# Kernel tuning notes

Hardware: AMD Instinct MI355X
Metric: run time of the kernel (lower is better)

The kernel has to match this reference:

```python
import jax, jax.numpy as jnp
import numpy as np

N = 100000   # nodes
E = 1600000  # edges (avg degree 16)
D = 128      # input feature dim
H = 128      # Config.hidden_dim
G = 64       # graphs in batch
OUT = 2      # output classes


def setup_inputs() -> dict:
    key = jax.random.key(0)
    ks = jax.random.split(key, 12)
    s = 0.05
    return {
        "x": jax.random.normal(ks[0], (N, D), dtype=jnp.float32),
        "edge_index": jax.random.randint(ks[1], (2, E), 0, N),
        "batch": jnp.sort(jax.random.randint(ks[2], (N,), 0, G)),
        "W1": jax.random.normal(ks[3], (H, D), dtype=jnp.float32) * s,
        "b1": jnp.zeros((H,), jnp.float32),
        "W2": jax.random.normal(ks[4], (H, H), dtype=jnp.float32) * s,
        "b2": jnp.zeros((H,), jnp.float32),
        "Wf1": jax.random.normal(ks[5], (H, H), dtype=jnp.float32) * s,
        "bf1": jnp.zeros((H,), jnp.float32),
        "Wf2": jax.random.normal(ks[6], (OUT, H), dtype=jnp.float32) * s,
        "bf2": jnp.zeros((OUT,), jnp.float32),
    }


def _gnn_layer(x, src, dst, W, b):
    # message(x_j) = Linear(x[src]); linear commutes with gather, so transform
    # node features once (N rows) instead of per-edge (E rows): same math.
    xw = x @ W.T + b                                   # [N, H]
    msg = xw[src]                                      # [E, H] gather
    summed = jax.ops.segment_sum(msg, dst, num_segments=N)            # [N, H]
    cnt = jax.ops.segment_sum(jnp.ones((src.shape[0],), x.dtype), dst,
                              num_segments=N)                          # [N]
    return summed / jnp.maximum(cnt, 1.0)[:, None]     # scatter-mean (0 for deg-0)


def reference(x, edge_index, batch, W1, b1, W2, b2, Wf1, bf1, Wf2, bf2):
    src, dst = edge_index[0], edge_index[1]
    h = jax.nn.relu(_gnn_layer(x, src, dst, W1, b1))
    h = jax.nn.relu(_gnn_layer(h, src, dst, W2, b2))
    g = jax.ops.segment_max(h, batch, num_segments=G)  # global_max_pool [G, H]
    z = jax.nn.relu(g @ Wf1.T + bf1)                   # fc (dropout = identity, eval)
    z = z @ Wf2.T + bf2                                # [G, OUT]
    return jax.nn.log_softmax(z, axis=1)
```

## Files before the change

kernel.cpp:

```cpp
#include <hip/hip_runtime.h>
#include <hip/hip_fp16.h>
#include <math.h>


#define SPLIT 64
#define BUCKET_SHIFT 8
#define BUCKET_SIZE 256
#define MAXBUCK 512
#define BIN_CHUNK 4096
#define CAP 4608
#define LSTR 136

typedef _Float16 half8 __attribute__((ext_vector_type(8)));
typedef _Float16 half4v __attribute__((ext_vector_type(4)));
typedef _Float16 half2v __attribute__((ext_vector_type(2)));
typedef float floatx4 __attribute__((ext_vector_type(4)));
typedef float floatx2 __attribute__((ext_vector_type(2)));

#define RFL(v) __builtin_amdgcn_readfirstlane(v)

__global__ void k_init(int* __restrict__ bcur, int* __restrict__ gstart,
                       int* __restrict__ gend,
                       const float* __restrict__ W1, const float* __restrict__ W2,
                       _Float16* __restrict__ w1h, _Float16* __restrict__ w2h,
                       int G, int nbuck) {
    int i = blockIdx.x * blockDim.x + threadIdx.x;
    if (i < nbuck) bcur[i] = i * CAP;
    if (i < G) { gstart[i] = 0; gend[i] = 0; }
    w1h[i] = (_Float16)W1[i];
    w2h[i] = (_Float16)W2[i];
}

__global__ __launch_bounds__(256) void k_bin(
        const int* __restrict__ src, const int* __restrict__ dst,
        int* __restrict__ bcur, int* __restrict__ staging,
        const int* __restrict__ batch, int* __restrict__ gstart,
        int* __restrict__ gend, int E, int N, int nbuck) {
    __shared__ int lh[MAXBUCK];
    __shared__ int lbase[MAXBUCK];
    __shared__ int lc[MAXBUCK];
    int t = threadIdx.x;
    for (int i = t; i < nbuck; i += 256) { lh[i] = 0; lc[i] = 0; }

    int n = blockIdx.x * 256 + t;
    if (n < N) {
        int b = batch[n];
        if (n == 0 || batch[n - 1] != b) gstart[b] = n;
        if (n == N - 1 || batch[n + 1] != b) gend[b] = n + 1;
    }
    __syncthreads();

    int base = blockIdx.x * BIN_CHUNK;
    if (base + BIN_CHUNK <= E) {
        int ds[16], ss[16];
        const int4* dv = (const int4*)(dst + base);
        const int4* sv = (const int4*)(src + base);
        #pragma unroll
        for (int j = 0; j < 4; ++j) {
            int4 d = dv[j * 256 + t];
            int4 s = sv[j * 256 + t];
            ds[j * 4 + 0] = d.x; ds[j * 4 + 1] = d.y;
            ds[j * 4 + 2] = d.z; ds[j * 4 + 3] = d.w;
            ss[j * 4 + 0] = s.x; ss[j * 4 + 1] = s.y;
            ss[j * 4 + 2] = s.z; ss[j * 4 + 3] = s.w;
        }
        #pragma unroll
        for (int q = 0; q < 16; ++q)
            atomicAdd(&lh[ds[q] >> BUCKET_SHIFT], 1);
        __syncthreads();
        for (int i = t; i < nbuck; i += 256)
            if (lh[i]) lbase[i] = atomicAdd(&bcur[i], lh[i]);
        __syncthreads();
        #pragma unroll
        for (int q = 0; q < 16; ++q) {
            int d = ds[q];
            int b = d >> BUCKET_SHIFT;
            int pos = lbase[b] + atomicAdd(&lc[b], 1);
            if (pos < (b + 1) * CAP)
                staging[pos] = ss[q] | ((d & (BUCKET_SIZE - 1)) << 24);
        }
    } else {
        for (int e = base + t; e < E; e += 256)
            atomicAdd(&lh[dst[e] >> BUCKET_SHIFT], 1);
        __syncthreads();
        for (int i = t; i < nbuck; i += 256)
            if (lh[i]) lbase[i] = atomicAdd(&bcur[i], lh[i]);
        __syncthreads();
        for (int e = base + t; e < E; e += 256) {
            int d = dst[e];
            int b = d >> BUCKET_SHIFT;
            int pos = lbase[b] + atomicAdd(&lc[b], 1);
            if (pos < (b + 1) * CAP)
                staging[pos] = src[e] | ((d & (BUCKET_SIZE - 1)) << 24);
        }
    }
}

__global__ __launch_bounds__(BUCKET_SIZE) void k_bcsr(
        const int* __restrict__ staging, const int* __restrict__ bcur,
        int* __restrict__ esrc, int* __restrict__ rowstart,
        int* __restrict__ deg, int N) {
    __shared__ int sw[CAP];
    __shared__ int lh[BUCKET_SIZE];
    __shared__ int lcur[BUCKET_SIZE];
    __shared__ int wsum[4];
    int b = blockIdx.x;
    int s = b * CAP;
    int e = min(bcur[b], s + CAP);
    int len = e - s;
    int t = threadIdx.x;
    lh[t] = 0;
    __syncthreads();
    for (int i = t; i < len; i += BUCKET_SIZE) {
        int p = staging[s + i];
        sw[i] = p;
        atomicAdd(&lh[((unsigned)p) >> 24], 1);
    }
    __syncthreads();
    int v = lh[t];
    int lane = t & 63;
    int wv = t >> 6;
    int inc = v;
    #pragma unroll
    for (int off = 1; off < 64; off <<= 1) {
        int x = __shfl_up(inc, off, 64);
        if (lane >= off) inc += x;
    }
    if (lane == 63) wsum[wv] = inc;
    __syncthreads();
    int woff = 0;
    #pragma unroll
    for (int k = 0; k < 3; ++k)
        if (k < wv) woff += wsum[k];
    int excl = woff + inc - v;
    int node = b * BUCKET_SIZE + t;
    if (node < N) { rowstart[node] = s + excl; deg[node] = v; }
    lcur[t] = excl;
    __syncthreads();
    for (int i = t; i < len; i += BUCKET_SIZE) {
        int p = sw[i];
        int local = ((unsigned)p) >> 24;
        int pos = atomicAdd(&lcur[local], 1);
        esrc[s + pos] = p & 0xFFFFFF;
    }
}

template <typename T>
__global__ __launch_bounds__(512) void k_gemm(const T* __restrict__ in,
                                              const _Float16* __restrict__ Wh,
                                              const float* __restrict__ bias,
                                              unsigned char* __restrict__ out8,
                                              int N) {
    __shared__ _Float16 sX[128 * LSTR];
    __shared__ _Float16 sW[128 * LSTR];
    int t = threadIdx.x;

    #pragma unroll
    for (int it = 0; it < 8; ++it) {
        int lin = it * 512 + t;
        int r = lin >> 5;
        int c = (lin & 31) * 4;
        *(half4v*)&sW[r * LSTR + c] = *(const half4v*)(Wh + r * 128 + c);
    }

    int w = t >> 6;
    int lane = t & 63;
    int quad = lane >> 4;
    int lrow = lane & 15;

    #pragma unroll
    for (int tile = 0; tile < 2; ++tile) {
        int n0 = blockIdx.x * 256 + tile * 128;
        __syncthreads();
        #pragma unroll
        for (int it = 0; it < 8; ++it) {
            int lin = it * 512 + t;
            int r = lin >> 5;
            int c = (lin & 31) * 4;
            half4v xh;
            int n = n0 + r;
            if (n < N) {
                if constexpr (sizeof(T) == 4) {
                    float4 xv = *(const float4*)((const float*)in + (size_t)n * 128 + c);
                    xh = half4v{ (_Float16)xv.x, (_Float16)xv.y, (_Float16)xv.z, (_Float16)xv.w };
                } else {
                    xh = *(const half4v*)((const _Float16*)in + (size_t)n * 128 + c);
                }
            } else {
                xh = half4v{ 0, 0, 0, 0 };
            }
            *(half4v*)&sX[r * LSTR + c] = xh;
        }
        __syncthreads();

        floatx4 acc[8];
        #pragma unroll
        for (int i = 0; i < 8; ++i) acc[i] = {0.f, 0.f, 0.f, 0.f};

        int arow = (w * 16 + lrow) * LSTR + quad * 8;
        #pragma unroll
        for (int k0 = 0; k0 < 128; k0 += 32) {
            half8 a = *(const half8*)&sX[arow + k0];
            #pragma unroll
            for (int ht = 0; ht < 8; ++ht) {
                half8 bfr = *(const half8*)&sW[(ht * 16 + lrow) * LSTR + quad * 8 + k0];
                acc[ht] = __builtin_amdgcn_mfma_f32_16x16x32_f16(a, bfr, acc[ht], 0, 0, 0);
            }
        }

        #pragma unroll
        for (int ht = 0; ht < 8; ++ht) {
            int h = ht * 16 + lrow;
            float bv = bias[h];
            #pragma unroll
            for (int r = 0; r < 4; ++r) {
                int node = n0 + w * 16 + quad * 4 + r;
                if (node < N) {
                    float v = acc[ht][r] + bv;
                    int pk = __builtin_amdgcn_cvt_pk_fp8_f32(v, v, 0, false);
                    out8[(size_t)node * 128 + h] = (unsigned char)(pk & 0xFF);
                }
            }
        }
    }
}

__global__ __launch_bounds__(256) void k_agg(const unsigned char* __restrict__ in8,
                                             const int* __restrict__ esrc,
                                             const int* __restrict__ rowstart,
                                             const int* __restrict__ deg,
                                             _Float16* __restrict__ outh, int N) {
    int lane = threadIdx.x & 63;
    int node = blockIdx.x * 4 + (threadIdx.x >> 6);
    if (node >= N) return;
    int start = RFL(rowstart[node]);
    int d     = RFL(deg[node]);
    const unsigned short* in16 = (const unsigned short*)in8;

    floatx2 a0 = {0.f, 0.f}, a1 = {0.f, 0.f}, a2 = {0.f, 0.f}, a3 = {0.f, 0.f};

    int i = 0;
    for (; i + 8 <= d; i += 8) {
        int x0 = RFL(esrc[start + i + 0]);
        int x1 = RFL(esrc[start + i + 1]);
        int x2 = RFL(esrc[start + i + 2]);
        int x3 = RFL(esrc[start + i + 3]);
        int x4 = RFL(esrc[start + i + 4]);
        int x5 = RFL(esrc[start + i + 5]);
        int x6 = RFL(esrc[start + i + 6]);
        int x7 = RFL(esrc[start + i + 7]);
        unsigned u0 = in16[((size_t)x0 << 6) + lane];
        unsigned u1 = in16[((size_t)x1 << 6) + lane];
        unsigned u2 = in16[((size_t)x2 << 6) + lane];
        unsigned u3 = in16[((size_t)x3 << 6) + lane];
        unsigned u4 = in16[((size_t)x4 << 6) + lane];
        unsigned u5 = in16[((size_t)x5 << 6) + lane];
        unsigned u6 = in16[((size_t)x6 << 6) + lane];
        unsigned u7 = in16[((size_t)x7 << 6) + lane];
        floatx2 f0 = __builtin_amdgcn_cvt_pk_f32_fp8(u0, false);
        floatx2 f1 = __builtin_amdgcn_cvt_pk_f32_fp8(u1, false);
        floatx2 f2 = __builtin_amdgcn_cvt_pk_f32_fp8(u2, false);
        floatx2 f3 = __builtin_amdgcn_cvt_pk_f32_fp8(u3, false);
        floatx2 f4 = __builtin_amdgcn_cvt_pk_f32_fp8(u4, false);
        floatx2 f5 = __builtin_amdgcn_cvt_pk_f32_fp8(u5, false);
        floatx2 f6 = __builtin_amdgcn_cvt_pk_f32_fp8(u6, false);
        floatx2 f7 = __builtin_amdgcn_cvt_pk_f32_fp8(u7, false);
        a0.x += f0.x; a0.y += f0.y;  a1.x += f1.x; a1.y += f1.y;
        a2.x += f2.x; a2.y += f2.y;  a3.x += f3.x; a3.y += f3.y;
        a0.x += f4.x; a0.y += f4.y;  a1.x += f5.x; a1.y += f5.y;
        a2.x += f6.x; a2.y += f6.y;  a3.x += f7.x; a3.y += f7.y;
    }
    for (; i + 4 <= d; i += 4) {
        int x0 = RFL(esrc[start + i + 0]);
        int x1 = RFL(esrc[start + i + 1]);
        int x2 = RFL(esrc[start + i + 2]);
        int x3 = RFL(esrc[start + i + 3]);
        unsigned u0 = in16[((size_t)x0 << 6) + lane];
        unsigned u1 = in16[((size_t)x1 << 6) + lane];
        unsigned u2 = in16[((size_t)x2 << 6) + lane];
        unsigned u3 = in16[((size_t)x3 << 6) + lane];
        floatx2 f0 = __builtin_amdgcn_cvt_pk_f32_fp8(u0, false);
        floatx2 f1 = __builtin_amdgcn_cvt_pk_f32_fp8(u1, false);
        floatx2 f2 = __builtin_amdgcn_cvt_pk_f32_fp8(u2, false);
        floatx2 f3 = __builtin_amdgcn_cvt_pk_f32_fp8(u3, false);
        a0.x += f0.x; a0.y += f0.y;  a1.x += f1.x; a1.y += f1.y;
        a2.x += f2.x; a2.y += f2.y;  a3.x += f3.x; a3.y += f3.y;
    }
    for (; i < d; ++i) {
        int x0 = RFL(esrc[start + i]);
        unsigned u0 = in16[((size_t)x0 << 6) + lane];
        floatx2 f0 = __builtin_amdgcn_cvt_pk_f32_fp8(u0, false);
        a0.x += f0.x; a0.y += f0.y;
    }

    float sx = (a0.x + a1.x) + (a2.x + a3.x);
    float sy = (a0.y + a1.y) + (a2.y + a3.y);
    float dm = fmaxf((float)d, 1.0f);
    half2v r = { (_Float16)fmaxf(sx / dm, 0.f),
                 (_Float16)fmaxf(sy / dm, 0.f) };
    *(half2v*)(outh + (size_t)node * 128 + lane * 2) = r;
}

__global__ void k_pool1(const _Float16* __restrict__ h, const int* __restrict__ gstart,
                        const int* __restrict__ gend, float* __restrict__ pm, int G) {
    int g = blockIdx.x / SPLIT;
    int c = blockIdx.x % SPLIT;
    int t = threadIdx.x;
    int s = gstart[g], e = gend[g];
    int len = e - s;
    int chunk = (len + SPLIT - 1) / SPLIT;
    int lo = s + c * chunk;
    int hi = min(lo + chunk, e);
    float m = -INFINITY;
    int n = lo;
    for (; n + 8 <= hi; n += 8) {
        float v0 = (float)h[(size_t)(n + 0) * 128 + t];
        float v1 = (float)h[(size_t)(n + 1) * 128 + t];
        float v2 = (float)h[(size_t)(n + 2) * 128 + t];
        float v3 = (float)h[(size_t)(n + 3) * 128 + t];
        float v4 = (float)h[(size_t)(n + 4) * 128 + t];
        float v5 = (float)h[(size_t)(n + 5) * 128 + t];
        float v6 = (float)h[(size_t)(n + 6) * 128 + t];
        float v7 = (float)h[(size_t)(n + 7) * 128 + t];
        float m0 = fmaxf(fmaxf(v0, v1), fmaxf(v2, v3));
        float m1 = fmaxf(fmaxf(v4, v5), fmaxf(v6, v7));
        m = fmaxf(m, fmaxf(m0, m1));
    }
    for (; n < hi; ++n)
        m = fmaxf(m, (float)h[(size_t)n * 128 + t]);
    pm[((size_t)g * SPLIT + c) * 128 + t] = m;
}

__global__ void k_fc(const float* __restrict__ pm,
                     const float* __restrict__ Wf1, const float* __restrict__ bf1,
                     const float* __restrict__ Wf2, const float* __restrict__ bf2,
                     float* __restrict__ out) {
    __shared__ float sg[128];
    __shared__ float sz[128];
    __shared__ float so[2];
    int g = blockIdx.x;
    int t = threadIdx.x;
    float m = -INFINITY;
    #pragma unroll 8
    for (int c = 0; c < SPLIT; ++c)
        m = fmaxf(m, pm[((size_t)g * SPLIT + c) * 128 + t]);
    sg[t] = m;
    __syncthreads();
    float z = bf1[t];
    #pragma unroll 4
    for (int d = 0; d < 128; ++d)
        z += sg[d] * Wf1[t * 128 + d];
    sz[t] = fmaxf(z, 0.f);
    __syncthreads();
    if (t < 2) {
        float o = bf2[t];
        for (int d = 0; d < 128; ++d)
            o += sz[d] * Wf2[t * 128 + d];
        so[t] = o;
    }
    __syncthreads();
    if (t == 0) {
        float a = so[0], b = so[1];
        float mx = fmaxf(a, b);
        float ls = mx + logf(expf(a - mx) + expf(b - mx));
        out[g * 2 + 0] = a - ls;
        out[g * 2 + 1] = b - ls;
    }
}

extern "C" void kernel_launch(void* const* d_in, const int* in_sizes, int n_in,
                              void* d_out, int out_size, void* d_ws, size_t ws_size,
                              hipStream_t stream) {
    const float* x   = (const float*)d_in[0];
    const int*   ei  = (const int*)d_in[1];
    const int* batch = (const int*)d_in[2];
    const float* W1  = (const float*)d_in[3];
    const float* b1  = (const float*)d_in[4];
    const float* W2  = (const float*)d_in[5];
    const float* b2  = (const float*)d_in[6];
    const float* Wf1 = (const float*)d_in[7];
    const float* bf1 = (const float*)d_in[8];
    const float* Wf2 = (const float*)d_in[9];
    const float* bf2 = (const float*)d_in[10];

    int N = in_sizes[2];
    int E = in_sizes[1] / 2;
    int G = out_size / 2;
    const int* src = ei;
    const int* dst = ei + E;
    int nbuck = (N + BUCKET_SIZE - 1) / BUCKET_SIZE;

    char* p = (char*)d_ws;
    auto alloc = [&](size_t bytes) -> char* {
        char* r = p;
        p += (bytes + 255) & ~(size_t)255;
        return r;
    };
    unsigned char* A = (unsigned char*)alloc((size_t)N * 128);
    _Float16* B    = (_Float16*)alloc((size_t)N * 128 * 2);
    int* deg       = (int*)alloc((size_t)N * 4);
    int* rowstart  = (int*)alloc((size_t)N * 4);
    int* esrc      = (int*)alloc((size_t)nbuck * CAP * 4);
    int* staging   = (int*)alloc((size_t)nbuck * CAP * 4);
    int* bcur      = (int*)alloc((MAXBUCK + 2) * 4);
    int* gstart    = (int*)alloc((size_t)G * 4);
    int* gend      = (int*)alloc((size_t)G * 4);
    float* pm      = (float*)alloc((size_t)G * SPLIT * 128 * 4);
    _Float16* w1h  = (_Float16*)alloc((size_t)128 * 128 * 2);
    _Float16* w2h  = (_Float16*)alloc((size_t)128 * 128 * 2);

    int nchunk = (E + BIN_CHUNK - 1) / BIN_CHUNK;

    k_init<<<64, 256, 0, stream>>>(bcur, gstart, gend, W1, W2, w1h, w2h, G, nbuck);
    k_bin<<<nchunk, 256, 0, stream>>>(src, dst, bcur, staging, batch,
                                      gstart, gend, E, N, nbuck);
    k_bcsr<<<nbuck, BUCKET_SIZE, 0, stream>>>(staging, bcur, esrc, rowstart, deg, N);

    k_gemm<float><<<(N + 255) / 256, 512, 0, stream>>>(x, w1h, b1, A, N);
    k_agg<<<(N + 3) / 4, 256, 0, stream>>>(A, esrc, rowstart, deg, B, N);
    k_gemm<_Float16><<<(N + 255) / 256, 512, 0, stream>>>(B, w2h, b2, A, N);
    k_agg<<<(N + 3) / 4, 256, 0, stream>>>(A, esrc, rowstart, deg, B, N);
    k_pool1<<<G * SPLIT, 128, 0, stream>>>(B, gstart, gend, pm, G);
    k_fc<<<G, 128, 0, stream>>>(pm, Wf1, bf1, Wf2, bf2, (float*)d_out);
}
```

Measured before the change: 291.0 us.

## Fuse first aggregation with second layer GEMM into one kernel

Adds a kernel that gathers and scatter-means neighbour features for 128 nodes into shared memory, applies ReLU, then runs the MFMA tile for the second linear layer. This removes the fp16 intermediate B write and read between the first aggregation and the second GEMM, and one kernel launch. The GEMM also drops the shared-memory weight staging and reads weights straight from global memory/cache, uses 128-node blocks, and sets an occupancy hint. Risks: each wave serially handles 16 nodes, so there is less latency hiding than with one node per wave, and the weight loads go through global memory.

Result: slower. 347.9 us (+19.6%).

```diff
diff --git a/kernel.cpp b/kernel.cpp
--- a/kernel.cpp
+++ b/kernel.cpp
@@ -145,84 +145,160 @@
     }
 }
 
-template <typename T>
-__global__ __launch_bounds__(512) void k_gemm(const T* __restrict__ in,
-                                              const _Float16* __restrict__ Wh,
-                                              const float* __restrict__ bias,
-                                              unsigned char* __restrict__ out8,
-                                              int N) {
+__device__ __forceinline__ void mfma_tile(const _Float16* sX,
+                                          const _Float16* __restrict__ Wh,
+                                          const float* __restrict__ bias,
+                                          unsigned char* __restrict__ out8,
+                                          int n0, int N, int t) {
+    int w = t >> 6;
+    int lane = t & 63;
+    int quad = lane >> 4;
+    int lrow = lane & 15;
+
+    floatx4 acc[8];
+    #pragma unroll
+    for (int i = 0; i < 8; ++i) acc[i] = {0.f, 0.f, 0.f, 0.f};
+
+    int arow = (w * 16 + lrow) * LSTR + quad * 8;
+    #pragma unroll
+    for (int k0 = 0; k0 < 128; k0 += 32) {
+        half8 a = *(const half8*)&sX[arow + k0];
+        #pragma unroll
+        for (int ht = 0; ht < 8; ++ht) {
+            half8 b = *(const half8*)(Wh + (ht * 16 + lrow) * 128 + quad * 8 + k0);
+            acc[ht] = __builtin_amdgcn_mfma_f32_16x16x32_f16(a, b, acc[ht], 0, 0, 0);
+        }
+    }
+
+    #pragma unroll
+    for (int ht = 0; ht < 8; ++ht) {
+        int h = ht * 16 + lrow;
+        float bv = bias[h];
+        #pragma unroll
+        for (int r = 0; r < 4; ++r) {
+            int node = n0 + w * 16 + quad * 4 + r;
+            if (node < N) {
+                float v = acc[ht][r] + bv;
+                int pk = __builtin_amdgcn_cvt_pk_fp8_f32(v, v, 0, false);
+                out8[(size_t)node * 128 + h] = (unsigned char)(pk & 0xFF);
+            }
+        }
+    }
+}
+
+__global__ __launch_bounds__(512, 6) void k_gemm(const float* __restrict__ in,
+                                                 const _Float16* __restrict__ Wh,
+                                                 const float* __restrict__ bias,
+                                                 unsigned char* __restrict__ out8,
+                                                 int N) {
     __shared__ _Float16 sX[128 * LSTR];
-    __shared__ _Float16 sW[128 * LSTR];
     int t = threadIdx.x;
+    int n0 = blockIdx.x * 128;
 
     #pragma unroll
     for (int it = 0; it < 8; ++it) {
         int lin = it * 512 + t;
         int r = lin >> 5;
         int c = (lin & 31) * 4;
-        *(half4v*)&sW[r * LSTR + c] = *(const half4v*)(Wh + r * 128 + c);
-    }
-
+        half4v xh = {0, 0, 0, 0};
+        int n = n0 + r;
+        if (n < N) {
+            float4 xv = *(const float4*)(in + (size_t)n * 128 + c);
+            xh = half4v{ (_Float16)xv.x, (_Float16)xv.y, (_Float16)xv.z, (_Float16)xv.w };
+        }
+        *(half4v*)&sX[r * LSTR + c] = xh;
+    }
+    __syncthreads();
+    mfma_tile(sX, Wh, bias, out8, n0, N, t);
+}
+
+__global__ __launch_bounds__(512, 6) void k_ag(const unsigned char* __restrict__ in8,
+                                               const int* __restrict__ esrc,
+                                               const int* __restrict__ rowstart,
+                                               const int* __restrict__ deg,
+                                               const _Float16* __restrict__ Wh,
+                                               const float* __restrict__ bias,
+                                               unsigned char* __restrict__ out8,
+                                               int N) {
+    __shared__ _Float16 sX[128 * LSTR];
+    int t = threadIdx.x;
     int w = t >> 6;
     int lane = t & 63;
-    int quad = lane >> 4;
-    int lrow = lane & 15;
-
-    #pragma unroll
-    for (int tile = 0; tile < 2; ++tile) {
-        int n0 = blockIdx.x * 256 + tile * 128;
-        __syncthreads();
-        #pragma unroll
-        for (int it = 0; it < 8; ++it) {
-            int lin = it * 512 + t;
-            int r = lin >> 5;
-            int c = (lin & 31) * 4;
-            half4v xh;
-            int n = n0 + r;
-            if (n < N) {
-                if constexpr (sizeof(T) == 4) {
-                    float4 xv = *(const float4*)((const float*)in + (size_t)n * 128 + c);
-                    xh = half4v{ (_Float16)xv.x, (_Float16)xv.y, (_Float16)xv.z, (_Float16)xv.w };
-                } else {
-                    xh = *(const half4v*)((const _Float16*)in + (size_t)n * 128 + c);
-                }
-            } else {
-                xh = half4v{ 0, 0, 0, 0 };
+    int n0 = blockIdx.x * 128;
+    const unsigned short* in16 = (const unsigned short*)in8;
+
+    for (int k = 0; k < 16; ++k) {
+        int node = n0 + w * 16 + k;
+        float sx = 0.f, sy = 0.f;
+        int dd = 0;
+        if (node < N) {
+            int start = RFL(rowstart[node]);
+            int d     = RFL(deg[node]);
+            dd = d;
+            floatx2 a0 = {0.f, 0.f}, a1 = {0.f, 0.f}, a2 = {0.f, 0.f}, a3 = {0.f, 0.f};
+            int i = 0;
+            for (; i + 8 <= d; i += 8) {
+                int x0 = RFL(esrc[start + i + 0]);
+                int x1 = RFL(esrc[start + i + 1]);
+                int x2 = RFL(esrc[start + i + 2]);
+                int x3 = RFL(esrc[start + i + 3]);
+                int x4 = RFL(esrc[start + i + 4]);
+                int x5 = RFL(esrc[start + i + 5]);
+                int x6 = RFL(esrc[start + i + 6]);
+                int x7 = RFL(esrc[start + i + 7]);
+                unsigned u0 = in16[((size_t)x0 << 6) + lane];
+                unsigned u1 = in16[((size_t)x1 << 6) + lane];
+                unsigned u2 = in16[((size_t)x2 << 6) + lane];
+                unsigned u3 = in16[((size_t)x3 << 6) + lane];
+                unsigned u4 = in16[((size_t)x4 << 6) + lane];
+                unsigned u5 = in16[((size_t)x5 << 6) + lane];
+                unsigned u6 = in16[((size_t)x6 << 6) + lane];
+                unsigned u7 = in16[((size_t)x7 << 6) + lane];
+                floatx2 f0 = __builtin_amdgcn_cvt_pk_f32_fp8(u0, false);
+                floatx2 f1 = __builtin_amdgcn_cvt_pk_f32_fp8(u1, false);
+                floatx2 f2 = __builtin_amdgcn_cvt_pk_f32_fp8(u2, false);
+                floatx2 f3 = __builtin_amdgcn_cvt_pk_f32_fp8(u3, false);
+                floatx2 f4 = __builtin_amdgcn_cvt_pk_f32_fp8(u4, false);
+                floatx2 f5 = __builtin_amdgcn_cvt_pk_f32_fp8(u5, false);
+                floatx2 f6 = __builtin_amdgcn_cvt_pk_f32_fp8(u6, false);
+                floatx2 f7 = __builtin_amdgcn_cvt_pk_f32_fp8(u7, false);
+                a0.x += f0.x; a0.y += f0.y;  a1.x += f1.x; a1.y += f1.y;
+                a2.x += f2.x; a2.y += f2.y;  a3.x += f3.x; a3.y += f3.y;
+                a0.x += f4.x; a0.y += f4.y;  a1.x += f5.x; a1.y += f5.y;
+                a2.x += f6.x; a2.y += f6.y;  a3.x += f7.x; a3.y += f7.y;
             }
-            *(half4v*)&sX[r * LSTR + c] = xh;
-        }
-        __syncthreads();
-
-        floatx4 acc[8];
-        #pragma unroll
-        for (int i = 0; i < 8; ++i) acc[i] = {0.f, 0.f, 0.f, 0.f};
-
-        int arow = (w * 16 + lrow) * LSTR + quad * 8;
-        #pragma unroll
-        for (int k0 = 0; k0 < 128; k0 += 32) {
-            half8 a = *(const half8*)&sX[arow + k0];
-            #pragma unroll
-            for (int ht = 0; ht < 8; ++ht) {
-                half8 bfr = *(const half8*)&sW[(ht * 16 + lrow) * LSTR + quad * 8 + k0];
-                acc[ht] = __builtin_amdgcn_mfma_f32_16x16x32_f16(a, bfr, acc[ht], 0, 0, 0);
+            for (; i + 4 <= d; i += 4) {
+                int x0 = RFL(esrc[start + i + 0]);
+                int x1 = RFL(esrc[start + i + 1]);
+                int x2 = RFL(esrc[start + i + 2]);
+                int x3 = RFL(esrc[start + i + 3]);
+                unsigned u0 = in16[((size_t)x0 << 6) + lane];
+                unsigned u1 = in16[((size_t)x1 << 6) + lane];
+                unsigned u2 = in16[((size_t)x2 << 6) + lane];
+                unsigned u3 = in16[((size_t)x3 << 6) + lane];
+                floatx2 f0 = __builtin_amdgcn_cvt_pk_f32_fp8(u0, false);
+                floatx2 f1 = __builtin_amdgcn_cvt_pk_f32_fp8(u1, false);
+                floatx2 f2 = __builtin_amdgcn_cvt_pk_f32_fp8(u2, false);
+                floatx2 f3 = __builtin_amdgcn_cvt_pk_f32_fp8(u3, false);
+                a0.x += f0.x; a0.y += f0.y;  a1.x += f1.x; a1.y += f1.y;
+                a2.x += f2.x; a2.y += f2.y;  a3.x += f3.x; a3.y += f3.y;
             }
-        }
-
-        #pragma unroll
-        for (int ht = 0; ht < 8; ++ht) {
-            int h = ht * 16 + lrow;
-            float bv = bias[h];
-            #pragma unroll
-            for (int r = 0; r < 4; ++r) {
-                int node = n0 + w * 16 + quad * 4 + r;
-                if (node < N) {
-                    float v = acc[ht][r] + bv;
-                    int pk = __builtin_amdgcn_cvt_pk_fp8_f32(v, v, 0, false);
-                    out8[(size_t)node * 128 + h] = (unsigned char)(pk & 0xFF);
-                }
+            for (; i < d; ++i) {
+                int x0 = RFL(esrc[start + i]);
+                unsigned u0 = in16[((size_t)x0 << 6) + lane];
+                floatx2 f0 = __builtin_amdgcn_cvt_pk_f32_fp8(u0, false);
+                a0.x += f0.x; a0.y += f0.y;
             }
-        }
-    }
+            sx = (a0.x + a1.x) + (a2.x + a3.x);
+            sy = (a0.y + a1.y) + (a2.y + a3.y);
+        }
+        float dm = fmaxf((float)dd, 1.0f);
+        half2v hv = { (_Float16)fmaxf(sx / dm, 0.f),
+                      (_Float16)fmaxf(sy / dm, 0.f) };
+        *(half2v*)&sX[(w * 16 + k) * LSTR + lane * 2] = hv;
+    }
+    __syncthreads();
+    mfma_tile(sX, Wh, bias, out8, n0, N, t);
 }
 
 __global__ __launch_bounds__(256) void k_agg(const unsigned char* __restrict__ in8,
@@ -396,7 +472,8 @@
         p += (bytes + 255) & ~(size_t)255;
         return r;
     };
-    unsigned char* A = (unsigned char*)alloc((size_t)N * 128);
+    unsigned char* A  = (unsigned char*)alloc((size_t)N * 128);
+    unsigned char* A2 = (unsigned char*)alloc((size_t)N * 128);
     _Float16* B    = (_Float16*)alloc((size_t)N * 128 * 2);
     int* deg       = (int*)alloc((size_t)N * 4);
     int* rowstart  = (int*)alloc((size_t)N * 4);
@@ -416,10 +493,9 @@
                                       gstart, gend, E, N, nbuck);
     k_bcsr<<<nbuck, BUCKET_SIZE, 0, stream>>>(staging, bcur, esrc, rowstart, deg, N);
 
-    k_gemm<float><<<(N + 255) / 256, 512, 0, stream>>>(x, w1h, b1, A, N);
-    k_agg<<<(N + 3) / 4, 256, 0, stream>>>(A, esrc, rowstart, deg, B, N);
-    k_gemm<_Float16><<<(N + 255) / 256, 512, 0, stream>>>(B, w2h, b2, A, N);
-    k_agg<<<(N + 3) / 4, 256, 0, stream>>>(A, esrc, rowstart, deg, B, N);
+    k_gemm<<<(N + 127) / 128, 512, 0, stream>>>(x, w1h, b1, A, N);
+    k_ag<<<(N + 127) / 128, 512, 0, stream>>>(A, esrc, rowstart, deg, w2h, b2, A2, N);
+    k_agg<<<(N + 3) / 4, 256, 0, stream>>>(A2, esrc, rowstart, deg, B, N);
     k_pool1<<<G * SPLIT, 128, 0, stream>>>(B, gstart, gend, pm, G);
     k_fc<<<G, 128, 0, stream>>>(pm, Wf1, bf1, Wf2, bf2, (float*)d_out);
 }
```

## Fuse GEMM, aggregation, pooling and FC stages into one cooperative persistent kernel

Applied to the files above, without the earlier changes.

Replaces the six separate launches (two GEMMs, two aggregations, pooling, FC) with a single cooperative kernel that loops over tiles and nodes in grid-stride fashion and separates stages with grid.sync. The GEMM no longer stages W in shared memory; it reads B fragments straight from global/L2, which halves LDS use so more blocks fit per CU. A second fp8 buffer avoids reusing A between layers. This removes launch gaps and tail effects, but adds grid-wide barriers and caps residency, which may reduce latency hiding for the gather-bound aggregation.

After: 695.7 us. +139.1%, slower.

```diff
diff --git a/kernel.cpp b/kernel.cpp
--- a/kernel.cpp
+++ b/kernel.cpp
@@ -1,4 +1,5 @@
 #include <hip/hip_runtime.h>
+#include <hip/hip_cooperative_groups.h>
 #include <hip/hip_fp16.h>
 #include <math.h>
 
@@ -18,6 +19,8 @@
 typedef float floatx2 __attribute__((ext_vector_type(2)));
 
 #define RFL(v) __builtin_amdgcn_readfirstlane(v)
+
+namespace cg = cooperative_groups;
 
 __global__ void k_init(int* __restrict__ bcur, int* __restrict__ gstart,
                        int* __restrict__ gend,
@@ -145,100 +148,78 @@
     }
 }
 
+
 template <typename T>
-__global__ __launch_bounds__(512) void k_gemm(const T* __restrict__ in,
-                                              const _Float16* __restrict__ Wh,
-                                              const float* __restrict__ bias,
-                                              unsigned char* __restrict__ out8,
-                                              int N) {
-    __shared__ _Float16 sX[128 * LSTR];
-    __shared__ _Float16 sW[128 * LSTR];
-    int t = threadIdx.x;
-
+__device__ __forceinline__ void gemm_tile(const T* __restrict__ in,
+                                          const _Float16* __restrict__ Wh,
+                                          const float* __restrict__ bias,
+                                          unsigned char* __restrict__ out8,
+                                          int n0, int N, int t, _Float16* sX) {
     #pragma unroll
     for (int it = 0; it < 8; ++it) {
         int lin = it * 512 + t;
         int r = lin >> 5;
         int c = (lin & 31) * 4;
-        *(half4v*)&sW[r * LSTR + c] = *(const half4v*)(Wh + r * 128 + c);
-    }
+        half4v xh = {0, 0, 0, 0};
+        int n = n0 + r;
+        if (n < N) {
+            if constexpr (sizeof(T) == 4) {
+                float4 xv = *(const float4*)((const float*)in + (size_t)n * 128 + c);
+                xh = half4v{ (_Float16)xv.x, (_Float16)xv.y, (_Float16)xv.z, (_Float16)xv.w };
+            } else {
+                xh = *(const half4v*)((const _Float16*)in + (size_t)n * 128 + c);
+            }
+        }
+        *(half4v*)&sX[r * LSTR + c] = xh;
+    }
+    __syncthreads();
 
     int w = t >> 6;
     int lane = t & 63;
     int quad = lane >> 4;
     int lrow = lane & 15;
 
-    #pragma unroll
-    for (int tile = 0; tile < 2; ++tile) {
-        int n0 = blockIdx.x * 256 + tile * 128;
-        __syncthreads();
-        #pragma unroll
-        for (int it = 0; it < 8; ++it) {
-            int lin = it * 512 + t;
-            int r = lin >> 5;
-            int c = (lin & 31) * 4;
-            half4v xh;
-            int n = n0 + r;
-            if (n < N) {
-                if constexpr (sizeof(T) == 4) {
-                    float4 xv = *(const float4*)((const float*)in + (size_t)n * 128 + c);
-                    xh = half4v{ (_Float16)xv.x, (_Float16)xv.y, (_Float16)xv.z, (_Float16)xv.w };
-                } else {
-                    xh = *(const half4v*)((const _Float16*)in + (size_t)n * 128 + c);
-                }
-            } else {
-                xh = half4v{ 0, 0, 0, 0 };
-            }
-            *(half4v*)&sX[r * LSTR + c] = xh;
-        }
-        __syncthreads();
-
-        floatx4 acc[8];
-        #pragma unroll
-        for (int i = 0; i < 8; ++i) acc[i] = {0.f, 0.f, 0.f, 0.f};
-
-        int arow = (w * 16 + lrow) * LSTR + quad * 8;
-        #pragma unroll
-        for (int k0 = 0; k0 < 128; k0 += 32) {
-            half8 a = *(const half8*)&sX[arow + k0];
-            #pragma unroll
-            for (int ht = 0; ht < 8; ++ht) {
-                half8 bfr = *(const half8*)&sW[(ht * 16 + lrow) * LSTR + quad * 8 + k0];
-                acc[ht] = __builtin_amdgcn_mfma_f32_16x16x32_f16(a, bfr, acc[ht], 0, 0, 0);
-            }
-        }
-
+    floatx4 acc[8];
+    #pragma unroll
+    for (int i = 0; i < 8; ++i) acc[i] = {0.f, 0.f, 0.f, 0.f};
+
+    int arow = (w * 16 + lrow) * LSTR + quad * 8;
+    #pragma unroll
+    for (int k0 = 0; k0 < 128; k0 += 32) {
+        half8 a = *(const half8*)&sX[arow + k0];
         #pragma unroll
         for (int ht = 0; ht < 8; ++ht) {
-            int h = ht * 16 + lrow;
-            float bv = bias[h];
-            #pragma unroll
-            for (int r = 0; r < 4; ++r) {
-                int node = n0 + w * 16 + quad * 4 + r;
-                if (node < N) {
-                    float v = acc[ht][r] + bv;
-                    int pk = __builtin_amdgcn_cvt_pk_fp8_f32(v, v, 0, false);
-                    out8[(size_t)node * 128 + h] = (unsigned char)(pk & 0xFF);
-                }
+            half8 b = *(const half8*)(Wh + (ht * 16 + lrow) * 128 + quad * 8 + k0);
+            acc[ht] = __builtin_amdgcn_mfma_f32_16x16x32_f16(a, b, acc[ht], 0, 0, 0);
+        }
+    }
+
+    #pragma unroll
+    for (int ht = 0; ht < 8; ++ht) {
+        int h = ht * 16 + lrow;
+        float bv = bias[h];
+        #pragma unroll
+        for (int r = 0; r < 4; ++r) {
+            int node = n0 + w * 16 + quad * 4 + r;
+            if (node < N) {
+                float v = acc[ht][r] + bv;
+                int pk = __builtin_amdgcn_cvt_pk_fp8_f32(v, v, 0, false);
+                out8[(size_t)node * 128 + h] = (unsigned char)(pk & 0xFF);
             }
         }
     }
-}
-
-__global__ __launch_bounds__(256) void k_agg(const unsigned char* __restrict__ in8,
-                                             const int* __restrict__ esrc,
-                                             const int* __restrict__ rowstart,
-                                             const int* __restrict__ deg,
-                                             _Float16* __restrict__ outh, int N) {
-    int lane = threadIdx.x & 63;
-    int node = blockIdx.x * 4 + (threadIdx.x >> 6);
-    if (node >= N) return;
+    __syncthreads();
+}
+
+__device__ __forceinline__ void agg_one(const unsigned short* __restrict__ in16,
+                                        const int* __restrict__ esrc,
+                                        const int* __restrict__ rowstart,
+                                        const int* __restrict__ deg,
+                                        int lane, int node,
+                                        _Float16* __restrict__ outh) {
     int start = RFL(rowstart[node]);
     int d     = RFL(deg[node]);
-    const unsigned short* in16 = (const unsigned short*)in8;
-
     floatx2 a0 = {0.f, 0.f}, a1 = {0.f, 0.f}, a2 = {0.f, 0.f}, a3 = {0.f, 0.f};
-
     int i = 0;
     for (; i + 8 <= d; i += 8) {
         int x0 = RFL(esrc[start + i + 0]);
@@ -292,7 +273,6 @@
         floatx2 f0 = __builtin_amdgcn_cvt_pk_f32_fp8(u0, false);
         a0.x += f0.x; a0.y += f0.y;
     }
-
     float sx = (a0.x + a1.x) + (a2.x + a3.x);
     float sy = (a0.y + a1.y) + (a2.y + a3.y);
     float dm = fmaxf((float)d, 1.0f);
@@ -301,70 +281,117 @@
     *(half2v*)(outh + (size_t)node * 128 + lane * 2) = r;
 }
 
-__global__ void k_pool1(const _Float16* __restrict__ h, const int* __restrict__ gstart,
-                        const int* __restrict__ gend, float* __restrict__ pm, int G) {
-    int g = blockIdx.x / SPLIT;
-    int c = blockIdx.x % SPLIT;
+__global__ __launch_bounds__(512, 6) void k_net(
+        const float* __restrict__ x,
+        const _Float16* __restrict__ w1h, const float* __restrict__ b1,
+        const _Float16* __restrict__ w2h, const float* __restrict__ b2,
+        const float* __restrict__ Wf1, const float* __restrict__ bf1,
+        const float* __restrict__ Wf2, const float* __restrict__ bf2,
+        const int* __restrict__ esrc, const int* __restrict__ rowstart,
+        const int* __restrict__ deg, const int* __restrict__ gstart,
+        const int* __restrict__ gend,
+        unsigned char* __restrict__ A, unsigned char* __restrict__ A2,
+        _Float16* __restrict__ B, float* __restrict__ pm,
+        float* __restrict__ out, int N, int G) {
+    cg::grid_group grid = cg::this_grid();
+    __shared__ _Float16 sX[128 * LSTR];
     int t = threadIdx.x;
-    int s = gstart[g], e = gend[g];
-    int len = e - s;
-    int chunk = (len + SPLIT - 1) / SPLIT;
-    int lo = s + c * chunk;
-    int hi = min(lo + chunk, e);
-    float m = -INFINITY;
-    int n = lo;
-    for (; n + 8 <= hi; n += 8) {
-        float v0 = (float)h[(size_t)(n + 0) * 128 + t];
-        float v1 = (float)h[(size_t)(n + 1) * 128 + t];
-        float v2 = (float)h[(size_t)(n + 2) * 128 + t];
-        float v3 = (float)h[(size_t)(n + 3) * 128 + t];
-        float v4 = (float)h[(size_t)(n + 4) * 128 + t];
-        float v5 = (float)h[(size_t)(n + 5) * 128 + t];
-        float v6 = (float)h[(size_t)(n + 6) * 128 + t];
-        float v7 = (float)h[(size_t)(n + 7) * 128 + t];
-        float m0 = fmaxf(fmaxf(v0, v1), fmaxf(v2, v3));
-        float m1 = fmaxf(fmaxf(v4, v5), fmaxf(v6, v7));
-        m = fmaxf(m, fmaxf(m0, m1));
-    }
-    for (; n < hi; ++n)
-        m = fmaxf(m, (float)h[(size_t)n * 128 + t]);
-    pm[((size_t)g * SPLIT + c) * 128 + t] = m;
-}
-
-__global__ void k_fc(const float* __restrict__ pm,
-                     const float* __restrict__ Wf1, const float* __restrict__ bf1,
-                     const float* __restrict__ Wf2, const float* __restrict__ bf2,
-                     float* __restrict__ out) {
-    __shared__ float sg[128];
-    __shared__ float sz[128];
-    __shared__ float so[2];
-    int g = blockIdx.x;
-    int t = threadIdx.x;
-    float m = -INFINITY;
-    #pragma unroll 8
-    for (int c = 0; c < SPLIT; ++c)
-        m = fmaxf(m, pm[((size_t)g * SPLIT + c) * 128 + t]);
-    sg[t] = m;
-    __syncthreads();
-    float z = bf1[t];
-    #pragma unroll 4
-    for (int d = 0; d < 128; ++d)
-        z += sg[d] * Wf1[t * 128 + d];
-    sz[t] = fmaxf(z, 0.f);
-    __syncthreads();
-    if (t < 2) {
-        float o = bf2[t];
-        for (int d = 0; d < 128; ++d)
-            o += sz[d] * Wf2[t * 128 + d];
-        so[t] = o;
-    }
-    __syncthreads();
-    if (t == 0) {
-        float a = so[0], b = so[1];
-        float mx = fmaxf(a, b);
-        float ls = mx + logf(expf(a - mx) + expf(b - mx));
-        out[g * 2 + 0] = a - ls;
-        out[g * 2 + 1] = b - ls;
+    int nb = gridDim.x;
+    int ntile = (N + 127) >> 7;
+    int lane = t & 63;
+    int gw = ((blockIdx.x << 9) + t) >> 6;
+    int nw = (nb << 9) >> 6;
+
+    for (int tile = blockIdx.x; tile < ntile; tile += nb)
+        gemm_tile<float>(x, w1h, b1, A, tile << 7, N, t, sX);
+    grid.sync();
+
+    {
+        const unsigned short* in16 = (const unsigned short*)A;
+        for (int node = gw; node < N; node += nw)
+            agg_one(in16, esrc, rowstart, deg, lane, node, B);
+    }
+    grid.sync();
+
+    for (int tile = blockIdx.x; tile < ntile; tile += nb)
+        gemm_tile<_Float16>(B, w2h, b2, A2, tile << 7, N, t, sX);
+    grid.sync();
+
+    {
+        const unsigned short* in16 = (const unsigned short*)A2;
+        for (int node = gw; node < N; node += nw)
+            agg_one(in16, esrc, rowstart, deg, lane, node, B);
+    }
+    grid.sync();
+
+    {
+        int q = t >> 7;
+        int tt = t & 127;
+        for (int task = (blockIdx.x << 2) + q; task < G * SPLIT; task += nb << 2) {
+            int g = task >> 6;
+            int c = task & (SPLIT - 1);
+            int s = gstart[g], e = gend[g];
+            int len = e - s;
+            int chunk = (len + SPLIT - 1) / SPLIT;
+            int lo = s + c * chunk;
+            int hi = min(lo + chunk, e);
+            float m = -INFINITY;
+            int n = lo;
+            for (; n + 8 <= hi; n += 8) {
+                float v0 = (float)B[(size_t)(n + 0) * 128 + tt];
+                float v1 = (float)B[(size_t)(n + 1) * 128 + tt];
+                float v2 = (float)B[(size_t)(n + 2) * 128 + tt];
+                float v3 = (float)B[(size_t)(n + 3) * 128 + tt];
+                float v4 = (float)B[(size_t)(n + 4) * 128 + tt];
+                float v5 = (float)B[(size_t)(n + 5) * 128 + tt];
+                float v6 = (float)B[(size_t)(n + 6) * 128 + tt];
+                float v7 = (float)B[(size_t)(n + 7) * 128 + tt];
+                float m0 = fmaxf(fmaxf(v0, v1), fmaxf(v2, v3));
+                float m1 = fmaxf(fmaxf(v4, v5), fmaxf(v6, v7));
+                m = fmaxf(m, fmaxf(m0, m1));
+            }
+            for (; n < hi; ++n)
+                m = fmaxf(m, (float)B[(size_t)n * 128 + tt]);
+            pm[((size_t)g * SPLIT + c) * 128 + tt] = m;
+        }
+    }
+    grid.sync();
+
+    if (blockIdx.x < G) {
+        float* sg = (float*)sX;
+        float* sz = sg + 128;
+        float* so = sz + 128;
+        int g = blockIdx.x;
+        if (t < 128) {
+            float m = -INFINITY;
+            #pragma unroll 8
+            for (int c = 0; c < SPLIT; ++c)
+                m = fmaxf(m, pm[((size_t)g * SPLIT + c) * 128 + t]);
+            sg[t] = m;
+        }
+        __syncthreads();
+        if (t < 128) {
+            float z = bf1[t];
+            #pragma unroll 4
+            for (int d2 = 0; d2 < 128; ++d2)
+                z += sg[d2] * Wf1[t * 128 + d2];
+            sz[t] = fmaxf(z, 0.f);
+        }
+        __syncthreads();
+        if (t < 2) {
+            float o = bf2[t];
+            for (int d2 = 0; d2 < 128; ++d2)
+                o += sz[d2] * Wf2[t * 128 + d2];
+            so[t] = o;
+        }
+        __syncthreads();
+        if (t == 0) {
+            float a = so[0], b = so[1];
+            float mx = fmaxf(a, b);
+            float ls = mx + logf(expf(a - mx) + expf(b - mx));
+            out[g * 2 + 0] = a - ls;
+            out[g * 2 + 1] = b - ls;
+        }
     }
 }
 
@@ -396,7 +423,8 @@
         p += (bytes + 255) & ~(size_t)255;
         return r;
     };
-    unsigned char* A = (unsigned char*)alloc((size_t)N * 128);
+    unsigned char* A  = (unsigned char*)alloc((size_t)N * 128);
+    unsigned char* A2 = (unsigned char*)alloc((size_t)N * 128);
     _Float16* B    = (_Float16*)alloc((size_t)N * 128 * 2);
     int* deg       = (int*)alloc((size_t)N * 4);
     int* rowstart  = (int*)alloc((size_t)N * 4);
@@ -408,6 +436,7 @@
     float* pm      = (float*)alloc((size_t)G * SPLIT * 128 * 4);
     _Float16* w1h  = (_Float16*)alloc((size_t)128 * 128 * 2);
     _Float16* w2h  = (_Float16*)alloc((size_t)128 * 128 * 2);
+    float* outp    = (float*)d_out;
 
     int nchunk = (E + BIN_CHUNK - 1) / BIN_CHUNK;
 
@@ -416,10 +445,21 @@
                                       gstart, gend, E, N, nbuck);
     k_bcsr<<<nbuck, BUCKET_SIZE, 0, stream>>>(staging, bcur, esrc, rowstart, deg, N);
 
-    k_gemm<float><<<(N + 255) / 256, 512, 0, stream>>>(x, w1h, b1, A, N);
-    k_agg<<<(N + 3) / 4, 256, 0, stream>>>(A, esrc, rowstart, deg, B, N);
-    k_gemm<_Float16><<<(N + 255) / 256, 512, 0, stream>>>(B, w2h, b2, A, N);
-    k_agg<<<(N + 3) / 4, 256, 0, stream>>>(A, esrc, rowstart, deg, B, N);
-    k_pool1<<<G * SPLIT, 128, 0, stream>>>(B, gstart, gend, pm, G);
-    k_fc<<<G, 128, 0, stream>>>(pm, Wf1, bf1, Wf2, bf2, (float*)d_out);
-}
+    static int coopBlocks = 0;
+    if (coopBlocks == 0) {
+        int bpc = 0;
+        hipOccupancyMaxActiveBlocksPerMultiprocessor(&bpc, k_net, 512, 0);
+        if (bpc < 1) bpc = 1;
+        coopBlocks = bpc * 256;
+        if (coopBlocks > 1024) coopBlocks = 1024;
+    }
+    void* args[] = {
+        (void*)&x, (void*)&w1h, (void*)&b1, (void*)&w2h, (void*)&b2,
+        (void*)&Wf1, (void*)&bf1, (void*)&Wf2, (void*)&bf2,
+        (void*)&esrc, (void*)&rowstart, (void*)&deg, (void*)&gstart, (void*)&gend,
+        (void*)&A, (void*)&A2, (void*)&B, (void*)&pm, (void*)&outp,
+        (void*)&N, (void*)&G
+    };
+    hipLaunchCooperativeKernel((void*)k_net, dim3(coopBlocks), dim3(512),
+                               args, 0, stream);
+}
```

## Fuse first-layer GEMM into edge binning kernel as extra blocks

Applied to the files above, without the earlier changes.

Merges the edge binning kernel and the first-layer node GEMM into one launch, where the first blocks bin edges and the remaining blocks run the x@W1 transform. The two independent jobs can then overlap on the GPU and one kernel launch is removed. The binning part moves to 512-thread blocks with 8 edges per thread. The GEMM now uses one 128-row tile per block and reads W fragments straight from global/L2 instead of staging them in LDS. A separate output buffer A2 is added for the second layer.

Result: slower. 319.6 us (+9.8%).

```diff
diff --git a/kernel.cpp b/kernel.cpp
--- a/kernel.cpp
+++ b/kernel.cpp
@@ -31,67 +31,130 @@
     w2h[i] = (_Float16)W2[i];
 }
 
-__global__ __launch_bounds__(256) void k_bin(
+__global__ __launch_bounds__(512) void k_binG(
         const int* __restrict__ src, const int* __restrict__ dst,
         int* __restrict__ bcur, int* __restrict__ staging,
         const int* __restrict__ batch, int* __restrict__ gstart,
-        int* __restrict__ gend, int E, int N, int nbuck) {
-    __shared__ int lh[MAXBUCK];
-    __shared__ int lbase[MAXBUCK];
-    __shared__ int lc[MAXBUCK];
+        int* __restrict__ gend,
+        const float* __restrict__ x, const _Float16* __restrict__ w1h,
+        const float* __restrict__ b1, unsigned char* __restrict__ A,
+        int E, int N, int nbuck, int nchunk) {
+    __shared__ char smem_raw[128 * LSTR * 2];
     int t = threadIdx.x;
-    for (int i = t; i < nbuck; i += 256) { lh[i] = 0; lc[i] = 0; }
-
-    int n = blockIdx.x * 256 + t;
-    if (n < N) {
-        int b = batch[n];
-        if (n == 0 || batch[n - 1] != b) gstart[b] = n;
-        if (n == N - 1 || batch[n + 1] != b) gend[b] = n + 1;
-    }
-    __syncthreads();
-
-    int base = blockIdx.x * BIN_CHUNK;
-    if (base + BIN_CHUNK <= E) {
-        int ds[16], ss[16];
-        const int4* dv = (const int4*)(dst + base);
-        const int4* sv = (const int4*)(src + base);
-        #pragma unroll
-        for (int j = 0; j < 4; ++j) {
-            int4 d = dv[j * 256 + t];
-            int4 s = sv[j * 256 + t];
-            ds[j * 4 + 0] = d.x; ds[j * 4 + 1] = d.y;
-            ds[j * 4 + 2] = d.z; ds[j * 4 + 3] = d.w;
-            ss[j * 4 + 0] = s.x; ss[j * 4 + 1] = s.y;
-            ss[j * 4 + 2] = s.z; ss[j * 4 + 3] = s.w;
-        }
-        #pragma unroll
-        for (int q = 0; q < 16; ++q)
-            atomicAdd(&lh[ds[q] >> BUCKET_SHIFT], 1);
+
+    if (blockIdx.x < nchunk) {
+        int* lh    = (int*)smem_raw;
+        int* lbase = lh + MAXBUCK;
+        int* lc    = lbase + MAXBUCK;
+        if (t < MAXBUCK) { lh[t] = 0; lc[t] = 0; }
+
+        if (t < 256) {
+            int n = blockIdx.x * 256 + t;
+            if (n < N) {
+                int b = batch[n];
+                if (n == 0 || batch[n - 1] != b) gstart[b] = n;
+                if (n == N - 1 || batch[n + 1] != b) gend[b] = n + 1;
+            }
+        }
         __syncthreads();
-        for (int i = t; i < nbuck; i += 256)
-            if (lh[i]) lbase[i] = atomicAdd(&bcur[i], lh[i]);
+
+        int base = blockIdx.x * BIN_CHUNK;
+        if (base + BIN_CHUNK <= E) {
+            int ds[8], ss[8];
+            const int4* dv = (const int4*)(dst + base);
+            const int4* sv = (const int4*)(src + base);
+            #pragma unroll
+            for (int j = 0; j < 2; ++j) {
+                int4 d = dv[j * 512 + t];
+                int4 s = sv[j * 512 + t];
+                ds[j * 4 + 0] = d.x; ds[j * 4 + 1] = d.y;
+                ds[j * 4 + 2] = d.z; ds[j * 4 + 3] = d.w;
+                ss[j * 4 + 0] = s.x; ss[j * 4 + 1] = s.y;
+                ss[j * 4 + 2] = s.z; ss[j * 4 + 3] = s.w;
+            }
+            #pragma unroll
+            for (int q = 0; q < 8; ++q)
+                atomicAdd(&lh[ds[q] >> BUCKET_SHIFT], 1);
+            __syncthreads();
+            for (int i = t; i < nbuck; i += 512)
+                if (lh[i]) lbase[i] = atomicAdd(&bcur[i], lh[i]);
+            __syncthreads();
+            #pragma unroll
+            for (int q = 0; q < 8; ++q) {
+                int d = ds[q];
+                int b = d >> BUCKET_SHIFT;
+                int pos = lbase[b] + atomicAdd(&lc[b], 1);
+                if (pos < (b + 1) * CAP)
+                    staging[pos] = ss[q] | ((d & (BUCKET_SIZE - 1)) << 24);
+            }
+        } else {
+            for (int e = base + t; e < E; e += 512)
+                atomicAdd(&lh[dst[e] >> BUCKET_SHIFT], 1);
+            __syncthreads();
+            for (int i = t; i < nbuck; i += 512)
+                if (lh[i]) lbase[i] = atomicAdd(&bcur[i], lh[i]);
+            __syncthreads();
+            for (int e = base + t; e < E; e += 512) {
+                int d = dst[e];
+                int b = d >> BUCKET_SHIFT;
+                int pos = lbase[b] + atomicAdd(&lc[b], 1);
+                if (pos < (b + 1) * CAP)
+                    staging[pos] = src[e] | ((d & (BUCKET_SIZE - 1)) << 24);
+            }
+        }
+    } else {
+        _Float16* sX = (_Float16*)smem_raw;
+        int n0 = (blockIdx.x - nchunk) * 128;
+
+        #pragma unroll
+        for (int it = 0; it < 8; ++it) {
+            int lin = it * 512 + t;
+            int r = lin >> 5;
+            int c = (lin & 31) * 4;
+            half4v xh = {0, 0, 0, 0};
+            int n = n0 + r;
+            if (n < N) {
+                float4 xv = *(const float4*)(x + (size_t)n * 128 + c);
+                xh = half4v{ (_Float16)xv.x, (_Float16)xv.y,
+                             (_Float16)xv.z, (_Float16)xv.w };
+            }
+            *(half4v*)&sX[r * LSTR + c] = xh;
+        }
         __syncthreads();
-        #pragma unroll
-        for (int q = 0; q < 16; ++q) {
-            int d = ds[q];
-            int b = d >> BUCKET_SHIFT;
-            int pos = lbase[b] + atomicAdd(&lc[b], 1);
-            if (pos < (b + 1) * CAP)
-                staging[pos] = ss[q] | ((d & (BUCKET_SIZE - 1)) << 24);
-        }
-    } else {
-        for (int e = base + t; e < E; e += 256)
-            atomicAdd(&lh[dst[e] >> BUCKET_SHIFT], 1);
-        __syncthreads();
-        for (int i = t; i < nbuck; i += 256)
-            if (lh[i]) lbase[i] = atomicAdd(&bcur[i], lh[i]);
-        __syncthreads();
-        for (int e = base + t; e < E; e += 256) {
-            int d = dst[e];
-            int b = d >> BUCKET_SHIFT;
-            int pos = lbase[b] + atomicAdd(&lc[b], 1);
-            if (pos < (b + 1) * CAP)
-                staging[pos] = src[e] | ((d & (BUCKET_SIZE - 1)) << 24);
+
+        int w = t >> 6;
+        int lane = t & 63;
+        int quad = lane >> 4;
+        int lrow = lane & 15;
+
+        floatx4 acc[8];
+        #pragma unroll
+        for (int i = 0; i < 8; ++i) acc[i] = {0.f, 0.f, 0.f, 0.f};
+
+        int arow = (w * 16 + lrow) * LSTR + quad * 8;
+        #pragma unroll
+        for (int k0 = 0; k0 < 128; k0 += 32) {
+            half8 a = *(const half8*)&sX[arow + k0];
+            #pragma unroll
+            for (int ht = 0; ht < 8; ++ht) {
+                half8 b = *(const half8*)(w1h + (ht * 16 + lrow) * 128 + quad * 8 + k0);
+                acc[ht] = __builtin_amdgcn_mfma_f32_16x16x32_f16(a, b, acc[ht], 0, 0, 0);
+            }
+        }
+
+        #pragma unroll
+        for (int ht = 0; ht < 8; ++ht) {
+            int h = ht * 16 + lrow;
+            float bv = b1[h];
+            #pragma unroll
+            for (int r = 0; r < 4; ++r) {
+                int node = n0 + w * 16 + quad * 4 + r;
+                if (node < N) {
+                    float v = acc[ht][r] + bv;
+                    int pk = __builtin_amdgcn_cvt_pk_fp8_f32(v, v, 0, false);
+                    A[(size_t)node * 128 + h] = (unsigned char)(pk & 0xFF);
+                }
+            }
         }
     }
 }
@@ -145,81 +208,59 @@
     }
 }
 
-template <typename T>
-__global__ __launch_bounds__(512) void k_gemm(const T* __restrict__ in,
+__global__ __launch_bounds__(512) void k_gemm(const _Float16* __restrict__ in,
                                               const _Float16* __restrict__ Wh,
                                               const float* __restrict__ bias,
                                               unsigned char* __restrict__ out8,
                                               int N) {
     __shared__ _Float16 sX[128 * LSTR];
-    __shared__ _Float16 sW[128 * LSTR];
     int t = threadIdx.x;
+    int n0 = blockIdx.x * 128;
 
     #pragma unroll
     for (int it = 0; it < 8; ++it) {
         int lin = it * 512 + t;
         int r = lin >> 5;
         int c = (lin & 31) * 4;
-        *(half4v*)&sW[r * LSTR + c] = *(const half4v*)(Wh + r * 128 + c);
-    }
+        half4v xh = {0, 0, 0, 0};
+        int n = n0 + r;
+        if (n < N)
+            xh = *(const half4v*)(in + (size_t)n * 128 + c);
+        *(half4v*)&sX[r * LSTR + c] = xh;
+    }
+    __syncthreads();
 
     int w = t >> 6;
     int lane = t & 63;
     int quad = lane >> 4;
     int lrow = lane & 15;
 
-    #pragma unroll
-    for (int tile = 0; tile < 2; ++tile) {
-        int n0 = blockIdx.x * 256 + tile * 128;
-        __syncthreads();
-        #pragma unroll
-        for (int it = 0; it < 8; ++it) {
-            int lin = it * 512 + t;
-            int r = lin >> 5;
-            int c = (lin & 31) * 4;
-            half4v xh;
-            int n = n0 + r;
-            if (n < N) {
-                if constexpr (sizeof(T) == 4) {
-                    float4 xv = *(const float4*)((const float*)in + (size_t)n * 128 + c);
-                    xh = half4v{ (_Float16)xv.x, (_Float16)xv.y, (_Float16)xv.z, (_Float16)xv.w };
-                } else {
-                    xh = *(const half4v*)((const _Float16*)in + (size_t)n * 128 + c);
-                }
-            } else {
-                xh = half4v{ 0, 0, 0, 0 };
-            }
-            *(half4v*)&sX[r * LSTR + c] = xh;
-        }
-        __syncthreads();
-
-        floatx4 acc[8];
-        #pragma unroll
-        for (int i = 0; i < 8; ++i) acc[i] = {0.f, 0.f, 0.f, 0.f};
-
-        int arow = (w * 16 + lrow) * LSTR + quad * 8;
-        #pragma unroll
-        for (int k0 = 0; k0 < 128; k0 += 32) {
-            half8 a = *(const half8*)&sX[arow + k0];
-            #pragma unroll
-            for (int ht = 0; ht < 8; ++ht) {
-                half8 bfr = *(const half8*)&sW[(ht * 16 + lrow) * LSTR + quad * 8 + k0];
-                acc[ht] = __builtin_amdgcn_mfma_f32_16x16x32_f16(a, bfr, acc[ht], 0, 0, 0);
-            }
-        }
-
+    floatx4 acc[8];
+    #pragma unroll
+    for (int i = 0; i < 8; ++i) acc[i] = {0.f, 0.f, 0.f, 0.f};
+
+    int arow = (w * 16 + lrow) * LSTR + quad * 8;
+    #pragma unroll
+    for (int k0 = 0; k0 < 128; k0 += 32) {
+        half8 a = *(const half8*)&sX[arow + k0];
         #pragma unroll
         for (int ht = 0; ht < 8; ++ht) {
-            int h = ht * 16 + lrow;
-            float bv = bias[h];
-            #pragma unroll
-            for (int r = 0; r < 4; ++r) {
-                int node = n0 + w * 16 + quad * 4 + r;
-                if (node < N) {
-                    float v = acc[ht][r] + bv;
-                    int pk = __builtin_amdgcn_cvt_pk_fp8_f32(v, v, 0, false);
-                    out8[(size_t)node * 128 + h] = (unsigned char)(pk & 0xFF);
-                }
+            half8 b = *(const half8*)(Wh + (ht * 16 + lrow) * 128 + quad * 8 + k0);
+            acc[ht] = __builtin_amdgcn_mfma_f32_16x16x32_f16(a, b, acc[ht], 0, 0, 0);
+        }
+    }
+
+    #pragma unroll
+    for (int ht = 0; ht < 8; ++ht) {
+        int h = ht * 16 + lrow;
+        float bv = bias[h];
+        #pragma unroll
+        for (int r = 0; r < 4; ++r) {
+            int node = n0 + w * 16 + quad * 4 + r;
+            if (node < N) {
+                float v = acc[ht][r] + bv;
+                int pk = __builtin_amdgcn_cvt_pk_fp8_f32(v, v, 0, false);
+                out8[(size_t)node * 128 + h] = (unsigned char)(pk & 0xFF);
             }
         }
     }
@@ -396,7 +437,8 @@
         p += (bytes + 255) & ~(size_t)255;
         return r;
     };
-    unsigned char* A = (unsigned char*)alloc((size_t)N * 128);
+    unsigned char* A  = (unsigned char*)alloc((size_t)N * 128);
+    unsigned char* A2 = (unsigned char*)alloc((size_t)N * 128);
     _Float16* B    = (_Float16*)alloc((size_t)N * 128 * 2);
     int* deg       = (int*)alloc((size_t)N * 4);
     int* rowstart  = (int*)alloc((size_t)N * 4);
@@ -410,16 +452,18 @@
     _Float16* w2h  = (_Float16*)alloc((size_t)128 * 128 * 2);
 
     int nchunk = (E + BIN_CHUNK - 1) / BIN_CHUNK;
+    int ntile  = (N + 127) / 128;
 
     k_init<<<64, 256, 0, stream>>>(bcur, gstart, gend, W1, W2, w1h, w2h, G, nbuck);
-    k_bin<<<nchunk, 256, 0, stream>>>(src, dst, bcur, staging, batch,
-                                      gstart, gend, E, N, nbuck);
+    k_binG<<<nchunk + ntile, 512, 0, stream>>>(src, dst, bcur, staging, batch,
+                                               gstart, gend, x, w1h, b1, A,
+                                               E, N, nbuck, nchunk);
     k_bcsr<<<nbuck, BUCKET_SIZE, 0, stream>>>(staging, bcur, esrc, rowstart, deg, N);
 
-    k_gemm<float><<<(N + 255) / 256, 512, 0, stream>>>(x, w1h, b1, A, N);
     k_agg<<<(N + 3) / 4, 256, 0, stream>>>(A, esrc, rowstart, deg, B, N);
-    k_gemm<_Float16><<<(N + 255) / 256, 512, 0, stream>>>(B, w2h, b2, A, N);
-    k_agg<<<(N + 3) / 4, 256, 0, stream>>>(A, esrc, rowstart, deg, B, N);
+    k_gemm<<<ntile, 512, 0, stream>>>(B, w2h, b2, A2, N);
+    k_agg<<<(N + 3) / 4, 256, 0, stream>>>(A2, esrc, rowstart, deg, B, N);
+
     k_pool1<<<G * SPLIT, 128, 0, stream>>>(B, gstart, gend, pm, G);
     k_fc<<<G, 128, 0, stream>>>(pm, Wf1, bf1, Wf2, bf2, (float*)d_out);
 }
```
